# Optimization experiments

Hardware: AMD Instinct MI355X
Metric: run time of the kernel (lower is better)

## Reference

```python
import jax, jax.numpy as jnp
import numpy as np


def setup_inputs() -> dict:
    key = jax.random.key(0)
    k1, k2 = jax.random.split(key)
    B, H, W, C_IN, N_SUMS = 32, 128, 128, 32, 32
    # x holds log-probabilities coming from a previous SPN layer
    x = jax.random.normal(k1, (B, H, W, C_IN), dtype=jnp.float32)
    # logspace accumulators (raw logits; normalized via log_softmax over axis=2)
    accumulators = jax.random.normal(k2, (1, 1, C_IN, N_SUMS), dtype=jnp.float32)
    return {"x": x, "accumulators": accumulators}


def reference(x, accumulators):
    # log_softmax over the input-channel axis (axis=2 of [1,1,Cin,S])
    log_w = jax.nn.log_softmax(accumulators, axis=2)[0, 0]  # [Cin, S]
    # logconv1x1_2d: out[b,h,w,s] = logsumexp_c( x[b,h,w,c] + log_w[c,s] )
    # Implemented as a stable log-matmul to avoid materializing [B,H,W,C,S].
    m = jnp.max(x, axis=-1, keepdims=True)              # [B,H,W,1]
    p = jnp.exp(x - m)                                   # [B,H,W,Cin]
    w = jnp.exp(log_w)                                   # [Cin,S], entries <= 1
    out = m + jnp.log(jnp.einsum("bhwc,cs->bhws", p, w))  # [B,H,W,S]
    return out
```

## Files before the change

kernel.cpp:

```cpp
#include <hip/hip_runtime.h>
#include <hip/hip_bf16.h>
#include <math.h>

constexpr int CIN = 32;
constexpr int NS  = 32;

typedef __attribute__((ext_vector_type(4)))  float  f32x4;
typedef __attribute__((ext_vector_type(8)))  short  short8;
typedef __attribute__((ext_vector_type(16))) float  f32x16;

typedef __attribute__((address_space(1))) unsigned int gbl_u32;
typedef __attribute__((address_space(3))) unsigned int lds_u32;

__device__ __forceinline__ short f2bf(float f) {
    union { float f; unsigned u; } v; v.f = f;
    unsigned r = (v.u + 0x7FFFu + ((v.u >> 16) & 1u)) >> 16;
    return (short)r;
}

__device__ __forceinline__ unsigned pk2bf(float lo, float hi) {
    union { __hip_bfloat162 b; unsigned u; } cv;
    cv.b = __float22bfloat162_rn(float2{lo, hi});
    return cv.u;
}

__global__ __launch_bounds__(256)
void logconv_coal(const float* __restrict__ x,
                  const float* __restrict__ acc,
                  float* __restrict__ out) {
    __shared__ short8 wfrag[64][2];
    __shared__ __align__(16) char bufs[4][2][4096];

    const int lane = threadIdx.x & 63;
    const int wid  = threadIdx.x >> 6;
    const int r    = lane & 31;
    const int h    = lane >> 5;
    const int swz  = (lane * 16) ^ ((lane >> 3) << 4);
    const int rx   = (r & 7) << 4;

    const long tile0 = ((long)blockIdx.x * 4 + wid) * 4;
    const char* xbase = (const char*)x + tile0 * 4096;
    char*       obase = (char*)out      + tile0 * 4096;

#define GLD(T, BUF) do {                                                    \
        const char* s_ = xbase + (size_t)(T) * 4096;                        \
        char* l_ = (char*)&bufs[wid][BUF][0];                               \
        _Pragma("unroll")                                                   \
        for (int k_ = 0; k_ < 4; ++k_) {                                    \
            __builtin_amdgcn_global_load_lds(                               \
                (const gbl_u32*)(s_ + k_ * 1024 + swz),                     \
                (lds_u32*)(l_ + k_ * 1024), 16, 0, 0);                      \
        }                                                                   \
    } while (0)

#define VMWAIT(N) do {                                                     \
        asm volatile("s_waitcnt vmcnt(" #N ")" ::: "memory");               \
        __builtin_amdgcn_sched_barrier(0);                                  \
    } while (0)

    GLD(0, 0);
    GLD(1, 1);

    if (threadIdx.x < 32) {
        const int s = threadIdx.x;
        float a[CIN];
#pragma unroll
        for (int c = 0; c < CIN; ++c) a[c] = acc[c * NS + s];
        float wm = a[0];
#pragma unroll
        for (int c = 1; c < CIN; ++c) wm = fmaxf(wm, a[c]);
        float wsum = 0.f;
#pragma unroll
        for (int c = 0; c < CIN; ++c) { a[c] = __expf(a[c] - wm); wsum += a[c]; }
        float winv = 1.f / wsum;
        short8 f00, f01, f10, f11;
#pragma unroll
        for (int j = 0; j < 8; ++j) {
            f00[j] = f2bf(a[j]      * winv);
            f10[j] = f2bf(a[8 + j]  * winv);
            f01[j] = f2bf(a[16 + j] * winv);
            f11[j] = f2bf(a[24 + j] * winv);
        }
        wfrag[s][0]      = f00;
        wfrag[s][1]      = f01;
        wfrag[32 + s][0] = f10;
        wfrag[32 + s][1] = f11;
    }
    __syncthreads();

    const short8 w0 = wfrag[lane][0];
    const short8 w1 = wfrag[lane][1];

#define TILE(T, BUF) do {                                                   \
        char* b_ = (char*)&bufs[wid][BUF][0];                               \
        const f32x4 xa = *(const f32x4*)(b_ + r * 128 + ((32 * h)      ^ rx)); \
        const f32x4 xb = *(const f32x4*)(b_ + r * 128 + ((32 * h + 16) ^ rx)); \
        const f32x4 xc = *(const f32x4*)(b_ + r * 128 + ((64 + 32 * h) ^ rx)); \
        const f32x4 xd = *(const f32x4*)(b_ + r * 128 + ((80 + 32 * h) ^ rx)); \
        union { short8 s; unsigned u[4]; } pu0, pu1;                        \
        pu0.u[0] = pk2bf(__expf(xa.x), __expf(xa.y));                       \
        pu0.u[1] = pk2bf(__expf(xa.z), __expf(xa.w));                       \
        pu0.u[2] = pk2bf(__expf(xb.x), __expf(xb.y));                       \
        pu0.u[3] = pk2bf(__expf(xb.z), __expf(xb.w));                       \
        pu1.u[0] = pk2bf(__expf(xc.x), __expf(xc.y));                       \
        pu1.u[1] = pk2bf(__expf(xc.z), __expf(xc.w));                       \
        pu1.u[2] = pk2bf(__expf(xd.x), __expf(xd.y));                       \
        pu1.u[3] = pk2bf(__expf(xd.z), __expf(xd.w));                       \
        f32x16 accv;                                                        \
        _Pragma("unroll")                                                   \
        for (int i = 0; i < 16; ++i) accv[i] = 0.f;                         \
        accv = __builtin_amdgcn_mfma_f32_32x32x16_bf16(w0, pu0.s, accv, 0, 0, 0); \
        accv = __builtin_amdgcn_mfma_f32_32x32x16_bf16(w1, pu1.s, accv, 0, 0, 0); \
        f32x4 v0, v1, v2, v3;                                               \
        v0.x = __logf(accv[0]);  v0.y = __logf(accv[1]);                    \
        v0.z = __logf(accv[2]);  v0.w = __logf(accv[3]);                    \
        v1.x = __logf(accv[4]);  v1.y = __logf(accv[5]);                    \
        v1.z = __logf(accv[6]);  v1.w = __logf(accv[7]);                    \
        v2.x = __logf(accv[8]);  v2.y = __logf(accv[9]);                    \
        v2.z = __logf(accv[10]); v2.w = __logf(accv[11]);                   \
        v3.x = __logf(accv[12]); v3.y = __logf(accv[13]);                   \
        v3.z = __logf(accv[14]); v3.w = __logf(accv[15]);                   \
         \
          \
        *(f32x4*)(b_ + r * 128 + ((  0 + 16 * h) ^ rx)) = v0;               \
        *(f32x4*)(b_ + r * 128 + (( 32 + 16 * h) ^ rx)) = v1;               \
        *(f32x4*)(b_ + r * 128 + (( 64 + 16 * h) ^ rx)) = v2;               \
        *(f32x4*)(b_ + r * 128 + (( 96 + 16 * h) ^ rx)) = v3;               \
        asm volatile("" ::: "memory");   \
        const f32x4 o0 = *(const f32x4*)(b_ +    0 + swz);                  \
        const f32x4 o1 = *(const f32x4*)(b_ + 1024 + swz);                  \
        const f32x4 o2 = *(const f32x4*)(b_ + 2048 + swz);                  \
        const f32x4 o3 = *(const f32x4*)(b_ + 3072 + swz);                  \
        char* op_ = obase + (size_t)(T) * 4096 + lane * 16;                 \
        *(f32x4*)(op_ +    0) = o0;                                         \
        *(f32x4*)(op_ + 1024) = o1;                                         \
        *(f32x4*)(op_ + 2048) = o2;                                         \
        *(f32x4*)(op_ + 3072) = o3;                                         \
    } while (0)

    TILE(0, 0);
    GLD(2, 0);
    VMWAIT(8);
    TILE(1, 1);
    GLD(3, 1);
    VMWAIT(8);
    TILE(2, 0);
    VMWAIT(4);
    TILE(3, 1);

#undef GLD
#undef VMWAIT
#undef TILE
}

extern "C" void kernel_launch(void* const* d_in, const int* in_sizes, int n_in,
                              void* d_out, int out_size, void* d_ws, size_t ws_size,
                              hipStream_t stream) {
    const float* x   = (const float*)d_in[0];
    const float* acc = (const float*)d_in[1];
    float* out = (float*)d_out;

    int npix = in_sizes[0] / CIN;
    int grid = npix / (4 * 4 * 32);
    logconv_coal<<<grid, 256, 0, stream>>>(x, acc, out);
}
```

Before: 25.94 us.

## Use single-wave blocks with per-lane weight setup and triple-buffered prefetch

Each block now holds one 64-thread wave processing four tiles instead of four waves sharing a block. Each lane computes its own softmax weight fragment in registers, which removes the shared-memory weight table and the __syncthreads. Three LDS buffers let three tile loads be in flight before compute starts, with vmcnt waits retuned for the deeper pipeline. The cost is redundant softmax work in every lane and vmcnt counts that depend on exact counting of stores and the accumulator loads.

```diff
diff --git a/kernel.cpp b/kernel.cpp
--- a/kernel.cpp
+++ b/kernel.cpp
@@ -24,27 +24,25 @@
     return cv.u;
 }
 
-__global__ __launch_bounds__(256)
-void logconv_coal(const float* __restrict__ x,
+__global__ __launch_bounds__(64)
+void logconv_wave(const float* __restrict__ x,
                   const float* __restrict__ acc,
                   float* __restrict__ out) {
-    __shared__ short8 wfrag[64][2];
-    __shared__ __align__(16) char bufs[4][2][4096];
+    __shared__ __align__(16) char bufs[3][4096];
 
-    const int lane = threadIdx.x & 63;
-    const int wid  = threadIdx.x >> 6;
+    const int lane = threadIdx.x;
     const int r    = lane & 31;
     const int h    = lane >> 5;
     const int swz  = (lane * 16) ^ ((lane >> 3) << 4);
     const int rx   = (r & 7) << 4;
 
-    const long tile0 = ((long)blockIdx.x * 4 + wid) * 4;
+    const long tile0 = (long)blockIdx.x * 4;
     const char* xbase = (const char*)x + tile0 * 4096;
     char*       obase = (char*)out      + tile0 * 4096;
 
 #define GLD(T, BUF) do {                                                    \
         const char* s_ = xbase + (size_t)(T) * 4096;                        \
-        char* l_ = (char*)&bufs[wid][BUF][0];                               \
+        char* l_ = (char*)&bufs[BUF][0];                                    \
         _Pragma("unroll")                                                   \
         for (int k_ = 0; k_ < 4; ++k_) {                                    \
             __builtin_amdgcn_global_load_lds(                               \
@@ -58,41 +56,32 @@
         __builtin_amdgcn_sched_barrier(0);                                  \
     } while (0)
 
+    float a[CIN];
+#pragma unroll
+    for (int c = 0; c < CIN; ++c) a[c] = acc[c * NS + r];
+    __builtin_amdgcn_sched_barrier(0);
+
     GLD(0, 0);
     GLD(1, 1);
+    GLD(2, 2);
+    __builtin_amdgcn_sched_barrier(0);
 
-    if (threadIdx.x < 32) {
-        const int s = threadIdx.x;
-        float a[CIN];
+    float wm = a[0];
 #pragma unroll
-        for (int c = 0; c < CIN; ++c) a[c] = acc[c * NS + s];
-        float wm = a[0];
+    for (int c = 1; c < CIN; ++c) wm = fmaxf(wm, a[c]);
+    float wsum = 0.f;
 #pragma unroll
-        for (int c = 1; c < CIN; ++c) wm = fmaxf(wm, a[c]);
-        float wsum = 0.f;
+    for (int c = 0; c < CIN; ++c) { a[c] = __expf(a[c] - wm); wsum += a[c]; }
+    float winv = 1.f / wsum;
+    short8 w0, w1;
 #pragma unroll
-        for (int c = 0; c < CIN; ++c) { a[c] = __expf(a[c] - wm); wsum += a[c]; }
-        float winv = 1.f / wsum;
-        short8 f00, f01, f10, f11;
-#pragma unroll
-        for (int j = 0; j < 8; ++j) {
-            f00[j] = f2bf(a[j]      * winv);
-            f10[j] = f2bf(a[8 + j]  * winv);
-            f01[j] = f2bf(a[16 + j] * winv);
-            f11[j] = f2bf(a[24 + j] * winv);
-        }
-        wfrag[s][0]      = f00;
-        wfrag[s][1]      = f01;
-        wfrag[32 + s][0] = f10;
-        wfrag[32 + s][1] = f11;
+    for (int j = 0; j < 8; ++j) {
+        w0[j] = f2bf((h ? a[8 + j]  : a[j])      * winv);
+        w1[j] = f2bf((h ? a[24 + j] : a[16 + j]) * winv);
     }
-    __syncthreads();
-
-    const short8 w0 = wfrag[lane][0];
-    const short8 w1 = wfrag[lane][1];
 
 #define TILE(T, BUF) do {                                                   \
-        char* b_ = (char*)&bufs[wid][BUF][0];                               \
+        char* b_ = (char*)&bufs[BUF][0];                                    \
         const f32x4 xa = *(const f32x4*)(b_ + r * 128 + ((32 * h)      ^ rx)); \
         const f32x4 xb = *(const f32x4*)(b_ + r * 128 + ((32 * h + 16) ^ rx)); \
         const f32x4 xc = *(const f32x4*)(b_ + r * 128 + ((64 + 32 * h) ^ rx)); \
@@ -120,8 +109,6 @@
         v2.z = __logf(accv[10]); v2.w = __logf(accv[11]);                   \
         v3.x = __logf(accv[12]); v3.y = __logf(accv[13]);                   \
         v3.z = __logf(accv[14]); v3.w = __logf(accv[15]);                   \
-         \
-          \
         *(f32x4*)(b_ + r * 128 + ((  0 + 16 * h) ^ rx)) = v0;               \
         *(f32x4*)(b_ + r * 128 + (( 32 + 16 * h) ^ rx)) = v1;               \
         *(f32x4*)(b_ + r * 128 + (( 64 + 16 * h) ^ rx)) = v2;               \
@@ -138,15 +125,15 @@
         *(f32x4*)(op_ + 3072) = o3;                                         \
     } while (0)
 
+    VMWAIT(8);
     TILE(0, 0);
-    GLD(2, 0);
+    GLD(3, 0);
+    VMWAIT(12);
+    TILE(1, 1);
+    VMWAIT(12);
+    TILE(2, 2);
     VMWAIT(8);
-    TILE(1, 1);
-    GLD(3, 1);
-    VMWAIT(8);
-    TILE(2, 0);
-    VMWAIT(4);
-    TILE(3, 1);
+    TILE(3, 0);
 
 #undef GLD
 #undef VMWAIT
@@ -161,6 +148,6 @@
     float* out = (float*)d_out;
 
     int npix = in_sizes[0] / CIN;
-    int grid = npix / (4 * 4 * 32);
-    logconv_coal<<<grid, 256, 0, stream>>>(x, acc, out);
+    int grid = npix / (4 * 32);
+    logconv_wave<<<grid, 64, 0, stream>>>(x, acc, out);
 }
```

Result: slower. 27.84 us (+7.3%).
